# Kernel tuning notes

Hardware: AMD Instinct MI355X
Metric: run time of the kernel (lower is better)

The kernel has to match this reference:

```python
import jax, jax.numpy as jnp
from jax import lax
import numpy as np

H = 16        # hidden_size == input_size
L = 8         # num_layers


def _lstm_layer(x_seq, Wih, Whh, bih, bhh):
    # x_seq: [B, T, H] -> outputs [B, T, H]; PyTorch gate order i,f,g,o
    B = x_seq.shape[0]
    b = bih + bhh  # [4H]

    def step(carry, xt):
        h, c = carry
        gates = xt @ Wih.T + h @ Whh.T + b  # [B, 4H]
        i, f, g, o = jnp.split(gates, 4, axis=-1)
        c = jax.nn.sigmoid(f) * c + jax.nn.sigmoid(i) * jnp.tanh(g)
        h = jax.nn.sigmoid(o) * jnp.tanh(c)
        return (h, c), h

    h0 = jnp.zeros((B, H), x_seq.dtype)
    (_, _), hs = lax.scan(step, (h0, h0), jnp.swapaxes(x_seq, 0, 1))
    return jnp.swapaxes(hs, 0, 1)  # [B, T, H]


def setup_inputs() -> dict:
    key = jax.random.key(0)
    ks = jax.random.split(key, 9)
    s = 1.0 / np.sqrt(H)  # PyTorch default init scale
    x = jax.random.normal(ks[0], (2048, 512, H), dtype=jnp.float32)
    W_ih = jax.random.uniform(ks[1], (L, 4 * H, H), jnp.float32, -s, s)
    W_hh = jax.random.uniform(ks[2], (L, 4 * H, H), jnp.float32, -s, s)
    b_ih = jax.random.uniform(ks[3], (L, 4 * H), jnp.float32, -s, s)
    b_hh = jax.random.uniform(ks[4], (L, 4 * H), jnp.float32, -s, s)
    Wp = jax.random.uniform(ks[5], (3, H), jnp.float32, -s, s)
    bp = jax.random.uniform(ks[6], (3,), jnp.float32, -s, s)
    Wo = jax.random.uniform(ks[7], (3, H), jnp.float32, -s, s)
    bo = jax.random.uniform(ks[8], (3,), jnp.float32, -s, s)
    return {"x": x, "W_ih": W_ih, "W_hh": W_hh, "b_ih": b_ih, "b_hh": b_hh,
            "Wp": Wp, "bp": bp, "Wo": Wo, "bo": bo}


def reference(x, W_ih, W_hh, b_ih, b_hh, Wp, bp, Wo, bo):
    h = x
    for l in range(L):  # fixed small layer count
        h = _lstm_layer(h, W_ih[l], W_hh[l], b_ih[l], b_hh[l])
    last = h[:, -1, :]                       # [B, H]
    position = last @ Wp.T + bp              # [B, 3]
    orientation = jnp.tanh(last @ Wo.T + bo) # [B, 3]
    return jnp.concatenate((position, orientation), axis=1)  # [B, 6]
```

## Files before the change

kernel.cpp:

```cpp
#include <hip/hip_runtime.h>
#include <math.h>

typedef _Float16 f16x8 __attribute__((ext_vector_type(8)));
typedef _Float16 f16x2 __attribute__((ext_vector_type(2)));
typedef float    f32x4 __attribute__((ext_vector_type(4)));

constexpr int kT    = 512;
constexpr int kH    = 16;
constexpr int kL    = 8;
constexpr int kG    = 64;
constexpr int kNB   = 8;
constexpr int kPad  = 24;
constexpr int kRows = 9;
constexpr int kSlots= 16;
constexpr int kLyr  = kL + 1;
constexpr int kSE   = kLyr * kRows * kPad;
constexpr int kIters= 33;

constexpr float kL2E = 1.4426950408889634f;

__device__ __forceinline__ float ex2(float w)  { return __builtin_amdgcn_exp2f(w); }
__device__ __forceinline__ float rcp1p(float e){ return __builtin_amdgcn_rcpf(1.0f + e); }

__global__ __launch_bounds__(512, 2)
void lstm_bar(const float* __restrict__ x,
              const float* __restrict__ Wih, const float* __restrict__ Whh,
              const float* __restrict__ bih, const float* __restrict__ bhh,
              const float* __restrict__ Wp,  const float* __restrict__ bpos,
              const float* __restrict__ Wo,  const float* __restrict__ bori,
              float* __restrict__ out)
{
    const int tid  = threadIdx.x;
    const int l    = tid >> 6;
    const int lane = tid & 63;
    const int n    = lane & 15;
    const int q    = lane >> 4;
    const int bn   = n & 7;
    const bool bact = ((q >> 1) == (n >> 3));

    __shared__ __align__(16) _Float16 hb[kSlots][kLyr][kRows][kPad];

    {
        int* hz = (int*)&hb[0][0][0][0];
        for (int i = tid; i < (int)(sizeof(hb) / 4); i += 512) hz[i] = 0;
    }
    __syncthreads();

    const float asc = ((n & 3) == 2) ? (-2.0f * kL2E) : (-kL2E);
    auto loadA = [&](const float* W, int T) -> f16x8 {
        const int wrow = (n & 3) * 16 + (n >> 2) + 4 * (q >> 1) + 8 * T;
        const float* src = W + (size_t)l * kG * kH + wrow * kH;
        f16x8 a;
        #pragma unroll
        for (int j = 0; j < 8; ++j) {
            const int u = (q & 1) * 4 + (j >> 1) + 8 * (j & 1);
            a[j] = (_Float16)(asc * src[u]);
        }
        return a;
    };
    const f16x8 A1T0 = loadA(Wih, 0), A2T0 = loadA(Whh, 0);
    const f16x8 A1T1 = loadA(Wih, 1), A2T1 = loadA(Whh, 1);

    const int u0 = q + 4 * (n >> 3);
    f32x4 bias0, bias1;
    #pragma unroll
    for (int r = 0; r < 4; ++r) {
        const float sc = (r == 2) ? (-2.0f * kL2E) : (-kL2E);
        const int g0 = l * kG + r * 16 + u0;
        bias0[r] = sc * (bih[g0] + bhh[g0]);
        bias1[r] = sc * (bih[g0 + 8] + bhh[g0 + 8]);
    }

    const int boff = (bact ? bn * kPad : 8 * kPad) + (q & 1) * 8;
    const _Float16* b1b = &hb[0][l][0][0] + boff;
    _Float16* hw = &hb[0][l + 1][bn][2 * u0];
    _Float16* xw = &hb[0][0][lane >> 3][2 * (lane & 7)];

    const int bpbase = 4 * bn + 32 * (q & 1);
    const int mska   = bact ? -1 : 0;

    const int xa = lane & 7;
    const float* xg_ptr =
        x + ((size_t)(blockIdx.x * kNB + (lane >> 3)) * kT) * kH;
    float xa0 = 0.f, xa1 = 0.f, xb0 = 0.f, xb1 = 0.f;
    if (l == 0) {
        #pragma unroll
        for (int t = 0; t < 3; ++t) {
            f16x2 xp = { (_Float16)xg_ptr[t * kH + xa],
                         (_Float16)xg_ptr[t * kH + xa + 8] };
            *(f16x2*)(xw + ((t + 15) & 15) * kSE) = xp;
        }
        xa0 = xg_ptr[3 * kH + xa]; xa1 = xg_ptr[3 * kH + xa + 8];
        xb0 = xg_ptr[4 * kH + xa]; xb1 = xg_ptr[4 * kH + xa + 8];
    }
    __syncthreads();

    const f16x8 B1p = *(const f16x8*)(b1b + 15 * kSE);
    f32x4 dIn0 = __builtin_amdgcn_mfma_f32_16x16x32_f16(A1T0, B1p, bias0, 0, 0, 0);
    f32x4 dIn1 = __builtin_amdgcn_mfma_f32_16x16x32_f16(A1T1, B1p, bias1, 0, 0, 0);

    f16x8 B2r;
    #pragma unroll
    for (int j = 0; j < 8; ++j) B2r[j] = (_Float16)0.f;

    float c0 = 0.f, c1 = 0.f;
    const int tl = 2 * l;

    #pragma unroll 1
    for (int it = 0; it < kIters; ++it) {
        const int wb = it * 16;
        #pragma unroll
        for (int k = 0; k < 16; ++k) {
            const int w = wb + k;
            const int slotR = k * kSE;
            const int slotW = ((k + 1) & 15) * kSE;
            const int slotX = ((k + 2) & 15) * kSE;
            const bool active = ((unsigned)(w - tl) < (unsigned)kT);

            const f16x8 B1n = *(const f16x8*)(b1b + slotR);

            f32x4 d0 = __builtin_amdgcn_mfma_f32_16x16x32_f16(A2T0, B2r, dIn0, 0, 0, 0);
            f32x4 d1 = __builtin_amdgcn_mfma_f32_16x16x32_f16(A2T1, B2r, dIn1, 0, 0, 0);

            float h0, h1;
            {
                const float si = rcp1p(ex2(d0[0]));
                const float sf = rcp1p(ex2(d0[1]));
                const float sg = rcp1p(ex2(d0[2]));
                const float so = rcp1p(ex2(d0[3]));
                const float tgp = fmaf(-4.0f * kL2E, sg, 2.0f * kL2E);
                float cn = fmaf(sf, c0, si * tgp);
                cn = active ? cn : 0.0f;
                c0 = cn;
                h0 = so * fmaf(2.0f, rcp1p(ex2(cn)), -1.0f);
            }
            {
                const float si = rcp1p(ex2(d1[0]));
                const float sf = rcp1p(ex2(d1[1]));
                const float sg = rcp1p(ex2(d1[2]));
                const float so = rcp1p(ex2(d1[3]));
                const float tgp = fmaf(-4.0f * kL2E, sg, 2.0f * kL2E);
                float cn = fmaf(sf, c1, si * tgp);
                cn = active ? cn : 0.0f;
                c1 = cn;
                h1 = so * fmaf(2.0f, rcp1p(ex2(cn)), -1.0f);
            }

            f16x2 hp = { (_Float16)h0, (_Float16)h1 };
            union { f16x2 h; int i; } uh; uh.h = hp;
            const int hpi = uh.i;
            const int w0 = __builtin_amdgcn_ds_bpermute(bpbase      , hpi) & mska;
            const int w1 = __builtin_amdgcn_ds_bpermute(bpbase + 64 , hpi) & mska;
            const int w2 = __builtin_amdgcn_ds_bpermute(bpbase + 128, hpi) & mska;
            const int w3 = __builtin_amdgcn_ds_bpermute(bpbase + 192, hpi) & mska;

            *(f16x2*)(hw + slotW) = hp;

            union { int i[4]; f16x8 v; } ub;
            ub.i[0] = w0; ub.i[1] = w1; ub.i[2] = w2; ub.i[3] = w3;
            B2r = ub.v;

            if (l == 0) {
                f16x2 xp = { (_Float16)xa0, (_Float16)xa1 };
                *(f16x2*)(xw + slotX) = xp;
                xa0 = xb0; xa1 = xb1;
                int tn = w + 5; if (tn > kT - 1) tn = kT - 1;
                xb0 = xg_ptr[(size_t)tn * kH + xa];
                xb1 = xg_ptr[(size_t)tn * kH + xa + 8];
            }

            dIn0 = __builtin_amdgcn_mfma_f32_16x16x32_f16(A1T0, B1n, bias0, 0, 0, 0);
            dIn1 = __builtin_amdgcn_mfma_f32_16x16x32_f16(A1T1, B1n, bias1, 0, 0, 0);

            asm volatile("s_waitcnt lgkmcnt(0)\n\ts_barrier" ::: "memory");
        }
    }

    __syncthreads();

    if (l == kL - 1) {
        const int bb = lane >> 3;
        const int r  = lane & 7;
        if (r < 6) {
            const bool  isP   = (r < 3);
            const float* wrow = isP ? (Wp + r * kH) : (Wo + (r - 3) * kH);
            float acc = isP ? bpos[r] : bori[r - 3];
            #pragma unroll
            for (int u = 0; u < kH; ++u) {
                const int p = 2 * (u & 7) + (u >> 3);
                acc = fmaf((float)hb[14][kL][bb][p], wrow[u], acc);
            }
            if (!isP) acc = fmaf(2.0f, rcp1p(ex2(-2.0f * kL2E * acc)), -1.0f);
            out[(size_t)(blockIdx.x * kNB + bb) * 6 + r] = acc;
        }
    }
}

extern "C" void kernel_launch(void* const* d_in, const int* in_sizes, int n_in,
                              void* d_out, int out_size, void* d_ws, size_t ws_size,
                              hipStream_t stream) {
    const float* x    = (const float*)d_in[0];
    const float* Wih  = (const float*)d_in[1];
    const float* Whh  = (const float*)d_in[2];
    const float* bih  = (const float*)d_in[3];
    const float* bhh  = (const float*)d_in[4];
    const float* Wp   = (const float*)d_in[5];
    const float* bpos = (const float*)d_in[6];
    const float* Wo   = (const float*)d_in[7];
    const float* bori = (const float*)d_in[8];
    float* out = (float*)d_out;

    const int B = in_sizes[0] / (kT * kH);
    lstm_bar<<<dim3(B / kNB), dim3(512), 0, stream>>>(x, Wih, Whh, bih, bhh,
                                                      Wp, bpos, Wo, bori, out);
}
```

Baseline: 295.9 us.

## Split each LSTM layer across two waves, one per half of the hidden units

Each layer's gate computation is now split across two wavefronts (1024-thread blocks). Each wave handles 8 of the 16 hidden units, doing one recurrent and one input MFMA per step instead of two of each. The in-wave ds_bpermute exchange of h is dropped and h is read back from LDS by both waves. This is meant to halve the per-step serial latency on the critical path. In exchange it doubles the number of waves meeting at every block barrier and adds an LDS read of the recurrent operand each step.

```diff
diff --git a/kernel.cpp b/kernel.cpp
--- a/kernel.cpp
+++ b/kernel.cpp
@@ -2,7 +2,6 @@
 #include <math.h>
 
 typedef _Float16 f16x8 __attribute__((ext_vector_type(8)));
-typedef _Float16 f16x2 __attribute__((ext_vector_type(2)));
 typedef float    f32x4 __attribute__((ext_vector_type(4)));
 
 constexpr int kT    = 512;
@@ -22,8 +21,8 @@
 __device__ __forceinline__ float ex2(float w)  { return __builtin_amdgcn_exp2f(w); }
 __device__ __forceinline__ float rcp1p(float e){ return __builtin_amdgcn_rcpf(1.0f + e); }
 
-__global__ __launch_bounds__(512, 2)
-void lstm_bar(const float* __restrict__ x,
+__global__ __launch_bounds__(1024, 4)
+void lstm_w16(const float* __restrict__ x,
               const float* __restrict__ Wih, const float* __restrict__ Whh,
               const float* __restrict__ bih, const float* __restrict__ bhh,
               const float* __restrict__ Wp,  const float* __restrict__ bpos,
@@ -31,7 +30,9 @@
               float* __restrict__ out)
 {
     const int tid  = threadIdx.x;
-    const int l    = tid >> 6;
+    const int wv   = tid >> 6;
+    const int l    = wv >> 1;
+    const int T    = wv & 1;
     const int lane = tid & 63;
     const int n    = lane & 15;
     const int q    = lane >> 4;
@@ -42,135 +43,94 @@
 
     {
         int* hz = (int*)&hb[0][0][0][0];
-        for (int i = tid; i < (int)(sizeof(hb) / 4); i += 512) hz[i] = 0;
+        for (int i = tid; i < (int)(sizeof(hb) / 4); i += 1024) hz[i] = 0;
     }
     __syncthreads();
 
     const float asc = ((n & 3) == 2) ? (-2.0f * kL2E) : (-kL2E);
-    auto loadA = [&](const float* W, int T) -> f16x8 {
+    auto loadA = [&](const float* W) -> f16x8 {
         const int wrow = (n & 3) * 16 + (n >> 2) + 4 * (q >> 1) + 8 * T;
         const float* src = W + (size_t)l * kG * kH + wrow * kH;
         f16x8 a;
         #pragma unroll
-        for (int j = 0; j < 8; ++j) {
-            const int u = (q & 1) * 4 + (j >> 1) + 8 * (j & 1);
-            a[j] = (_Float16)(asc * src[u]);
-        }
+        for (int j = 0; j < 8; ++j)
+            a[j] = (_Float16)(asc * src[(q & 1) * 8 + j]);
         return a;
     };
-    const f16x8 A1T0 = loadA(Wih, 0), A2T0 = loadA(Whh, 0);
-    const f16x8 A1T1 = loadA(Wih, 1), A2T1 = loadA(Whh, 1);
+    const f16x8 A1 = loadA(Wih);
+    const f16x8 A2 = loadA(Whh);
 
-    const int u0 = q + 4 * (n >> 3);
-    f32x4 bias0, bias1;
+    const int u0 = q + 4 * (n >> 3) + 8 * T;
+    f32x4 bias;
     #pragma unroll
     for (int r = 0; r < 4; ++r) {
         const float sc = (r == 2) ? (-2.0f * kL2E) : (-kL2E);
         const int g0 = l * kG + r * 16 + u0;
-        bias0[r] = sc * (bih[g0] + bhh[g0]);
-        bias1[r] = sc * (bih[g0 + 8] + bhh[g0 + 8]);
+        bias[r] = sc * (bih[g0] + bhh[g0]);
     }
 
     const int boff = (bact ? bn * kPad : 8 * kPad) + (q & 1) * 8;
-    const _Float16* b1b = &hb[0][l][0][0] + boff;
-    _Float16* hw = &hb[0][l + 1][bn][2 * u0];
-    _Float16* xw = &hb[0][0][lane >> 3][2 * (lane & 7)];
+    const _Float16* b1b = &hb[0][l    ][0][0] + boff;
+    const _Float16* b2b = &hb[0][l + 1][0][0] + boff;
+    _Float16* hw = &hb[0][l + 1][bn][u0];
 
-    const int bpbase = 4 * bn + 32 * (q & 1);
-    const int mska   = bact ? -1 : 0;
-
-    const int xa = lane & 7;
+    const int xu = (lane & 7) + 8 * T;
+    _Float16* xw = &hb[0][0][lane >> 3][xu];
     const float* xg_ptr =
         x + ((size_t)(blockIdx.x * kNB + (lane >> 3)) * kT) * kH;
-    float xa0 = 0.f, xa1 = 0.f, xb0 = 0.f, xb1 = 0.f;
+    float xa = 0.f, xb = 0.f, xc = 0.f;
     if (l == 0) {
         #pragma unroll
-        for (int t = 0; t < 3; ++t) {
-            f16x2 xp = { (_Float16)xg_ptr[t * kH + xa],
-                         (_Float16)xg_ptr[t * kH + xa + 8] };
-            *(f16x2*)(xw + ((t + 15) & 15) * kSE) = xp;
-        }
-        xa0 = xg_ptr[3 * kH + xa]; xa1 = xg_ptr[3 * kH + xa + 8];
-        xb0 = xg_ptr[4 * kH + xa]; xb1 = xg_ptr[4 * kH + xa + 8];
+        for (int t = 0; t < 3; ++t)
+            *(xw + ((t + 15) & 15) * kSE) = (_Float16)xg_ptr[t * kH + xu];
+        xa = xg_ptr[3 * kH + xu];
+        xb = xg_ptr[4 * kH + xu];
+        xc = xg_ptr[5 * kH + xu];
     }
     __syncthreads();
 
     const f16x8 B1p = *(const f16x8*)(b1b + 15 * kSE);
-    f32x4 dIn0 = __builtin_amdgcn_mfma_f32_16x16x32_f16(A1T0, B1p, bias0, 0, 0, 0);
-    f32x4 dIn1 = __builtin_amdgcn_mfma_f32_16x16x32_f16(A1T1, B1p, bias1, 0, 0, 0);
+    f32x4 dIn = __builtin_amdgcn_mfma_f32_16x16x32_f16(A1, B1p, bias, 0, 0, 0);
 
-    f16x8 B2r;
-    #pragma unroll
-    for (int j = 0; j < 8; ++j) B2r[j] = (_Float16)0.f;
-
-    float c0 = 0.f, c1 = 0.f;
+    float c0 = 0.f;
     const int tl = 2 * l;
 
     #pragma unroll 1
     for (int it = 0; it < kIters; ++it) {
-        const int wb = it * 16;
+        const int sb = it * 16;
         #pragma unroll
         for (int k = 0; k < 16; ++k) {
-            const int w = wb + k;
+            const int s = sb + k;
             const int slotR = k * kSE;
             const int slotW = ((k + 1) & 15) * kSE;
             const int slotX = ((k + 2) & 15) * kSE;
-            const bool active = ((unsigned)(w - tl) < (unsigned)kT);
+            const bool active = ((unsigned)(s - tl) < (unsigned)kT);
 
+            const f16x8 B2r = *(const f16x8*)(b2b + slotR);
             const f16x8 B1n = *(const f16x8*)(b1b + slotR);
 
-            f32x4 d0 = __builtin_amdgcn_mfma_f32_16x16x32_f16(A2T0, B2r, dIn0, 0, 0, 0);
-            f32x4 d1 = __builtin_amdgcn_mfma_f32_16x16x32_f16(A2T1, B2r, dIn1, 0, 0, 0);
+            f32x4 d = __builtin_amdgcn_mfma_f32_16x16x32_f16(A2, B2r, dIn, 0, 0, 0);
 
-            float h0, h1;
-            {
-                const float si = rcp1p(ex2(d0[0]));
-                const float sf = rcp1p(ex2(d0[1]));
-                const float sg = rcp1p(ex2(d0[2]));
-                const float so = rcp1p(ex2(d0[3]));
-                const float tgp = fmaf(-4.0f * kL2E, sg, 2.0f * kL2E);
-                float cn = fmaf(sf, c0, si * tgp);
-                cn = active ? cn : 0.0f;
-                c0 = cn;
-                h0 = so * fmaf(2.0f, rcp1p(ex2(cn)), -1.0f);
-            }
-            {
-                const float si = rcp1p(ex2(d1[0]));
-                const float sf = rcp1p(ex2(d1[1]));
-                const float sg = rcp1p(ex2(d1[2]));
-                const float so = rcp1p(ex2(d1[3]));
-                const float tgp = fmaf(-4.0f * kL2E, sg, 2.0f * kL2E);
-                float cn = fmaf(sf, c1, si * tgp);
-                cn = active ? cn : 0.0f;
-                c1 = cn;
-                h1 = so * fmaf(2.0f, rcp1p(ex2(cn)), -1.0f);
+            const float si = rcp1p(ex2(d[0]));
+            const float sf = rcp1p(ex2(d[1]));
+            const float sg = rcp1p(ex2(d[2]));
+            const float so = rcp1p(ex2(d[3]));
+            const float tgp = fmaf(-4.0f * kL2E, sg, 2.0f * kL2E);
+            float cn = fmaf(sf, c0, si * tgp);
+            cn = active ? cn : 0.0f;
+            c0 = cn;
+            const float h0 = so * fmaf(2.0f, rcp1p(ex2(cn)), -1.0f);
+
+            *(hw + slotW) = (_Float16)h0;
+
+            if (l == 0) {
+                *(xw + slotX) = (_Float16)xa;
+                xa = xb; xb = xc;
+                int tn = s + 6; if (tn > kT - 1) tn = kT - 1;
+                xc = xg_ptr[(size_t)tn * kH + xu];
             }
 
-            f16x2 hp = { (_Float16)h0, (_Float16)h1 };
-            union { f16x2 h; int i; } uh; uh.h = hp;
-            const int hpi = uh.i;
-            const int w0 = __builtin_amdgcn_ds_bpermute(bpbase      , hpi) & mska;
-            const int w1 = __builtin_amdgcn_ds_bpermute(bpbase + 64 , hpi) & mska;
-            const int w2 = __builtin_amdgcn_ds_bpermute(bpbase + 128, hpi) & mska;
-            const int w3 = __builtin_amdgcn_ds_bpermute(bpbase + 192, hpi) & mska;
-
-            *(f16x2*)(hw + slotW) = hp;
-
-            union { int i[4]; f16x8 v; } ub;
-            ub.i[0] = w0; ub.i[1] = w1; ub.i[2] = w2; ub.i[3] = w3;
-            B2r = ub.v;
-
-            if (l == 0) {
-                f16x2 xp = { (_Float16)xa0, (_Float16)xa1 };
-                *(f16x2*)(xw + slotX) = xp;
-                xa0 = xb0; xa1 = xb1;
-                int tn = w + 5; if (tn > kT - 1) tn = kT - 1;
-                xb0 = xg_ptr[(size_t)tn * kH + xa];
-                xb1 = xg_ptr[(size_t)tn * kH + xa + 8];
-            }
-
-            dIn0 = __builtin_amdgcn_mfma_f32_16x16x32_f16(A1T0, B1n, bias0, 0, 0, 0);
-            dIn1 = __builtin_amdgcn_mfma_f32_16x16x32_f16(A1T1, B1n, bias1, 0, 0, 0);
+            dIn = __builtin_amdgcn_mfma_f32_16x16x32_f16(A1, B1n, bias, 0, 0, 0);
 
             asm volatile("s_waitcnt lgkmcnt(0)\n\ts_barrier" ::: "memory");
         }
@@ -178,7 +138,7 @@
 
     __syncthreads();
 
-    if (l == kL - 1) {
+    if (wv == 15) {
         const int bb = lane >> 3;
         const int r  = lane & 7;
         if (r < 6) {
@@ -186,10 +146,8 @@
             const float* wrow = isP ? (Wp + r * kH) : (Wo + (r - 3) * kH);
             float acc = isP ? bpos[r] : bori[r - 3];
             #pragma unroll
-            for (int u = 0; u < kH; ++u) {
-                const int p = 2 * (u & 7) + (u >> 3);
-                acc = fmaf((float)hb[14][kL][bb][p], wrow[u], acc);
-            }
+            for (int u = 0; u < kH; ++u)
+                acc = fmaf((float)hb[14][kL][bb][u], wrow[u], acc);
             if (!isP) acc = fmaf(2.0f, rcp1p(ex2(-2.0f * kL2E * acc)), -1.0f);
             out[(size_t)(blockIdx.x * kNB + bb) * 6 + r] = acc;
         }
@@ -211,6 +169,6 @@
     float* out = (float*)d_out;
 
     const int B = in_sizes[0] / (kT * kH);
-    lstm_bar<<<dim3(B / kNB), dim3(512), 0, stream>>>(x, Wih, Whh, bih, bhh,
-                                                      Wp, bpos, Wo, bori, out);
+    lstm_w16<<<dim3(B / kNB), dim3(1024), 0, stream>>>(x, Wih, Whh, bih, bhh,
+                                                       Wp, bpos, Wo, bori, out);
 }
```

New measurement: 280.1 us. 1.06x faster.
